# Performance work log

Hardware: AMD Instinct MI355X
Metric: run time of the kernel (lower is better)

The kernel has to match this reference:

```python
import jax, jax.numpy as jnp
import numpy as np

N, M, F0, FB, F, H, NC, NCONV = 60000, 12, 92, 41, 64, 128, 2000, 3
EPS = 1e-5


def setup_inputs() -> dict:
    key = jax.random.key(0)
    ks = jax.random.split(key, 12)
    s = 0.05
    return {
        "atom_fea": jax.random.normal(ks[0], (N, F0), jnp.float32),
        "nbr_fea": jax.random.normal(ks[1], (N, M, FB), jnp.float32),
        "nbr_fea_idx": jax.random.randint(ks[2], (N, M), 0, N),
        "crystal_atom_idx": jnp.sort(jax.random.randint(ks[3], (N,), 0, NC)),
        "W_emb": jax.random.normal(ks[4], (F0, F), jnp.float32) * s,
        "b_emb": jnp.zeros((F,), jnp.float32),
        "W_full": jax.random.normal(ks[5], (NCONV, 2 * F + FB, 2 * F), jnp.float32) * s,
        "b_full": jnp.zeros((NCONV, 2 * F), jnp.float32),
        "g1": jnp.ones((NCONV, 2 * F), jnp.float32),
        "be1": jnp.zeros((NCONV, 2 * F), jnp.float32),
        "g2": jnp.ones((NCONV, F), jnp.float32),
        "be2": jnp.zeros((NCONV, F), jnp.float32),
        "W_fc": jax.random.normal(ks[6], (F, H), jnp.float32) * s,
        "b_fc": jnp.zeros((H,), jnp.float32),
        "W_out": jax.random.normal(ks[7], (H, 1), jnp.float32) * s,
        "b_out": jnp.zeros((1,), jnp.float32),
    }


def _bn(x, g, b):
    # training-mode batch norm over leading (row) dim
    m = x.mean(axis=0)
    v = x.var(axis=0)
    return (x - m) * jax.lax.rsqrt(v + EPS) * g + b


def _conv_layer(x, nbr_fea, nbr_fea_idx, Wf, bf, g1, be1, g2, be2):
    n, m = nbr_fea_idx.shape
    f = x.shape[1]
    atom_nbr = x[nbr_fea_idx]  # (N, M, F) gather
    total = jnp.concatenate(
        [jnp.broadcast_to(x[:, None, :], (n, m, f)), atom_nbr, nbr_fea], axis=2
    )  # (N, M, 2F+FB)
    gated = total @ Wf + bf  # (N, M, 2F)
    gated = _bn(gated.reshape(-1, 2 * f), g1, be1).reshape(n, m, 2 * f)
    nbr_filter, nbr_core = jnp.split(gated, 2, axis=2)
    summed = jnp.sum(jax.nn.sigmoid(nbr_filter) * jax.nn.softplus(nbr_core), axis=1)
    summed = _bn(summed, g2, be2)
    return jax.nn.softplus(x + summed)


def reference(atom_fea, nbr_fea, nbr_fea_idx, crystal_atom_idx, W_emb, b_emb,
              W_full, b_full, g1, be1, g2, be2, W_fc, b_fc, W_out, b_out):
    x = atom_fea @ W_emb + b_emb  # (N, F)
    for i in range(NCONV):
        x = _conv_layer(x, nbr_fea, nbr_fea_idx, W_full[i], b_full[i],
                        g1[i], be1[i], g2[i], be2[i])
    # mean-pool atoms per crystal (segment mean)
    sums = jax.ops.segment_sum(x, crystal_atom_idx, num_segments=NC)
    cnt = jax.ops.segment_sum(jnp.ones((x.shape[0],), x.dtype), crystal_atom_idx,
                              num_segments=NC)
    crys = sums / jnp.maximum(cnt, 1.0)[:, None]  # (NC, F)
    crys = jax.nn.softplus(crys) @ W_fc + b_fc
    crys = jax.nn.softplus(crys)
    return crys @ W_out + b_out  # (NC, 1)
```

## Files before the change

### kernel.cpp

```cpp
#include <hip/hip_runtime.h>
#include <hip/hip_bf16.h>


#define NATOM 60000
#define MNBR  12
#define F0D   92
#define FBD   41
#define FD    64
#define F2D   128
#define NCRY  2000
#define HD    128
#define NSUP  15000
#define GS    132

#define OFF_X      0ull
#define OFF_XH     3840000ull
#define OFF_SUMMED 5760000ull
#define OFF_STATS  9600000ull
#define OFF_CRYS   9600384ull
#define OFF_CNT    9728384ull
#define OFF_WCONV  9730384ull
#define OFF_WBF    9811220ull
#define OFF_FLAG   9848084ull
#define WS_NEED_BYTES (9848085ull * 4ull)
#define OFF_BPAD   9848088ull
#define WS_FULL_BYTES ((OFF_BPAD + 17280000ull) * 4ull)

#define W_EMB_O  0
#define B_EMB_O  5888
#define W_FULL_O 5952
#define B_FULL_O 70848
#define G1_O     71232
#define BE1_O    71616
#define G2_O     72000
#define BE2_O    72192
#define W_FC_O   72384
#define B_FC_O   80576
#define W_OUT_O  80704
#define B_OUT_O  80832
#define WC_TOTAL 80833

typedef unsigned short u16;
typedef __attribute__((ext_vector_type(8))) short bf16x8;
typedef __attribute__((ext_vector_type(4))) float f32x4;

__device__ __forceinline__ float bf2f(u16 u){
  union { unsigned int i; float f; } v; v.i = ((unsigned int)u) << 16; return v.f;
}
__device__ __forceinline__ u16 f2bf(float f){
  union { float f; unsigned int i; } v; v.f = f;
  unsigned int x = v.i;
  return (u16)((x + 0x7FFFu + ((x >> 16) & 1u)) >> 16);
}
__device__ __forceinline__ float softplusf_(float x){
  return fmaxf(x, 0.f) + log1pf(expf(-fabsf(x)));
}
__device__ __forceinline__ float softplus_fast(float x){
  return fmaxf(x, 0.f) + __logf(1.f + __expf(-fabsf(x)));
}
__device__ __forceinline__ float sigmoid_fast(float x){
  return __builtin_amdgcn_rcpf(1.f + __expf(-x));
}

__global__ __launch_bounds__(64) void detect_kernel(
    const u16* __restrict__ data, int* __restrict__ flag){
  int tid = threadIdx.x;
  float v = bf2f(data[tid * 2]);
  float av = fabsf(v);
  bool sane = (av > 1e-6f) && (av < 100.f);
  unsigned long long m = __ballot(sane);
  if (tid == 0) *flag = (__popcll(m) >= 32) ? 1 : 0;
}

struct CvtArgs {
  const void* src[12];
  int start[13];
};

__global__ __launch_bounds__(256) void cvt_all_kernel(
    CvtArgs a, float* __restrict__ dst, const int* __restrict__ flag){
  int i = blockIdx.x * 256 + threadIdx.x;
  if (i >= WC_TOTAL) return;
  int r = 0;
  while (i >= a.start[r + 1]) r++;
  int rel = i - a.start[r];
  if (*flag) dst[i] = bf2f(((const u16*)a.src[r])[rel]);
  else       dst[i] = ((const float*)a.src[r])[rel];
}

__global__ __launch_bounds__(256) void build_bfrag(
    const float* __restrict__ wfull, u16* __restrict__ wbf){
  int t = blockIdx.x * 256 + threadIdx.x;
  if (t >= 3 * 6 * 8 * 64) return;
  int lane = t & 63, nt = (t >> 6) & 7, c = (t >> 9) % 6, layer = t / 3072;
  int q = lane >> 4, nloc = lane & 15;
  u16 vals[8];
  #pragma unroll
  for (int i = 0; i < 8; i++){
    int k = c * 32 + q * 8 + i;
    float v = (k < 169) ? wfull[layer * 169 * F2D + k * F2D + nt * 16 + nloc] : 0.f;
    vals[i] = f2bf(v);
  }
  *(uint4*)&wbf[(size_t)t * 8] = *(uint4*)vals;
}

__global__ __launch_bounds__(256) void bond_prep(
    const void* __restrict__ nbr_fea, u16* __restrict__ bond_pad,
    const int* __restrict__ flag){
  __shared__ __align__(16) char sm[7872];
  u16*   lb_u = (u16*)sm;
  float* lb_f = (float*)sm;
  int s = blockIdx.x, tid = threadIdx.x;
  const int isbf = *flag;
  if (isbf){
    const uint4* src = (const uint4*)((const u16*)nbr_fea + (size_t)s * 1968);
    if (tid < 246) ((uint4*)sm)[tid] = src[tid];
  } else {
    const uint4* src = (const uint4*)((const float*)nbr_fea + (size_t)s * 1968);
    for (int t = tid; t < 492; t += 256) ((uint4*)sm)[t] = src[t];
  }
  __syncthreads();
  uint4* outv = (uint4*)(bond_pad + (size_t)s * 2304);
  for (int slot = tid; slot < 288; slot += 256){
    int el = slot / 6, jj = slot - el * 6;
    u16 v[8];
    #pragma unroll
    for (int i = 0; i < 8; i++){
      int k = jj * 8 + i;
      v[i] = (k < FBD) ? (isbf ? lb_u[el * FBD + k] : f2bf(lb_f[el * FBD + k])) : (u16)0;
    }
    outv[slot] = *(uint4*)v;
  }
}

__global__ __launch_bounds__(256) void embed_kernel(
    const void* __restrict__ atom_fea, const float* __restrict__ W_emb,
    const float* __restrict__ b_emb, float* __restrict__ x,
    u16* __restrict__ xh, const int* __restrict__ flag){
  int tid = threadIdx.x;
  int n = blockIdx.x * 4 + (tid >> 6);
  int f = tid & 63;
  float acc = b_emb[f];
  if (*flag){
    const u16* arow = (const u16*)atom_fea + n * F0D;
    for (int k = 0; k < F0D; k++)
      acc = fmaf(bf2f(arow[k]), W_emb[k * FD + f], acc);
  } else {
    const float* arow = (const float*)atom_fea + n * F0D;
    for (int k = 0; k < F0D; k++)
      acc = fmaf(arow[k], W_emb[k * FD + f], acc);
  }
  x[n * FD + f] = acc;
  xh[n * FD + f] = f2bf(acc);
}

template<int ACT, int PAD>
__global__ __launch_bounds__(256, 3) void conv_mfma(
    const u16* __restrict__ xh, const void* __restrict__ nbr_fea,
    const u16* __restrict__ bond_pad,
    const int* __restrict__ nbr_idx, const u16* __restrict__ wbf_l,
    const float* __restrict__ bfull, const float* __restrict__ sum1,
    const float* __restrict__ sq1, const float* __restrict__ g1,
    const float* __restrict__ be1, float* __restrict__ summed,
    float* __restrict__ o_sum, float* __restrict__ o_sq,
    const int* __restrict__ flag){
  extern __shared__ char smem[];
  u16*   fragA = (u16*)smem;
  const int base_off = PAD ? 0 : 6144;
  float* gbuf  = (float*)(smem + base_off);
  float* redS  = ACT ? (gbuf + 48 * GS) : (float*)(smem + base_off);
  float* redQ  = redS + (ACT ? 64 : 128);

  const int tid = threadIdx.x;
  const int w = tid >> 6, lane = tid & 63;
  const int q = lane >> 4, nloc = lane & 15, q8 = q * 8;
  const int isbf = *flag;

  bf16x8 Bf[6][2];
  const bf16x8* Bv = (const bf16x8*)wbf_l;
  #pragma unroll
  for (int c = 0; c < 6; c++)
    #pragma unroll
    for (int t2 = 0; t2 < 2; t2++)
      Bf[c][t2] = Bv[(c * 8 + w * 2 + t2) * 64 + lane];
  float bias0 = bfull[w * 32 + nloc];
  float bias1 = bfull[w * 32 + 16 + nloc];

  float A0 = 0.f, B0 = 0.f, A1 = 0.f, B1 = 0.f;
  if (ACT){
    const float invR = 1.f / (float)(NATOM * MNBR);
    float m0 = sum1[lane] * invR;
    float v0 = fmaxf(sq1[lane] * invR - m0 * m0, 0.f);
    A0 = g1[lane] * rsqrtf(v0 + 1e-5f);  B0 = be1[lane] - m0 * A0;
    float m1 = sum1[64 + lane] * invR;
    float v1 = fmaxf(sq1[64 + lane] * invR - m1 * m1, 0.f);
    A1 = g1[64 + lane] * rsqrtf(v1 + 1e-5f);  B1 = be1[64 + lane] - m1 * A1;
  }
  float sAcc0 = 0.f, sAcc1 = 0.f, qAcc0 = 0.f, qAcc1 = 0.f;
  if (tid < (ACT ? 64 : 128)){ redS[tid] = 0.f; redQ[tid] = 0.f; }
  if (PAD && !ACT) ;

  const bf16x8* xv = (const bf16x8*)xh;
  const bf16x8 zero8 = {0,0,0,0,0,0,0,0};
  for (int s = blockIdx.x; s < NSUP; s += gridDim.x){
    int e0 = s * 48 + nloc;
    int nb0 = nbr_idx[e0], nb1 = nbr_idx[e0 + 16], nb2 = nbr_idx[e0 + 32];
    bf16x8 Af[3][6];
    if (PAD){
      #pragma unroll
      for (int et = 0; et < 3; et++){
        int nb = (et == 0) ? nb0 : (et == 1) ? nb1 : nb2;
        int na = s * 4 + (et * 16 + nloc) / 12;
        Af[et][0] = xv[na * 8 + q];
        Af[et][1] = xv[na * 8 + 4 + q];
        Af[et][2] = xv[nb * 8 + q];
        Af[et][3] = xv[nb * 8 + 4 + q];
        const bf16x8* bpv = (const bf16x8*)(bond_pad + (size_t)(e0 + et * 16) * 48);
        Af[et][4] = bpv[q];
        Af[et][5] = (q < 2) ? bpv[4 + q] : zero8;
      }
    } else {
      if (w < 3){
        size_t eg = (size_t)(s * 48 + w * 16 + nloc);
        u16 v4[8], v5[8];
        if (isbf){
          const u16* br = (const u16*)nbr_fea + eg * 41;
          #pragma unroll
          for (int i = 0; i < 8; i++) v4[i] = br[q8 + i];
          #pragma unroll
          for (int i = 0; i < 8; i++){
            int k5 = 32 + q8 + i;
            v5[i] = (k5 < 41) ? br[k5] : (u16)0;
          }
        } else {
          const float* br = (const float*)nbr_fea + eg * 41;
          #pragma unroll
          for (int i = 0; i < 8; i++) v4[i] = f2bf(br[q8 + i]);
          #pragma unroll
          for (int i = 0; i < 8; i++){
            int k5 = 32 + q8 + i;
            v5[i] = (k5 < 41) ? f2bf(br[k5]) : (u16)0;
          }
        }
        *(uint4*)&fragA[(w * 2 + 0) * 512 + lane * 8] = *(uint4*)v4;
        *(uint4*)&fragA[(w * 2 + 1) * 512 + lane * 8] = *(uint4*)v5;
      }
      __syncthreads();
      #pragma unroll
      for (int et = 0; et < 3; et++){
        int nb = (et == 0) ? nb0 : (et == 1) ? nb1 : nb2;
        int na = s * 4 + (et * 16 + nloc) / 12;
        Af[et][0] = xv[na * 8 + q];
        Af[et][1] = xv[na * 8 + 4 + q];
        Af[et][2] = xv[nb * 8 + q];
        Af[et][3] = xv[nb * 8 + 4 + q];
        Af[et][4] = *(bf16x8*)&fragA[(et * 2 + 0) * 512 + lane * 8];
        Af[et][5] = *(bf16x8*)&fragA[(et * 2 + 1) * 512 + lane * 8];
      }
    }
    #pragma unroll
    for (int et = 0; et < 3; et++){
      #pragma unroll
      for (int t2 = 0; t2 < 2; t2++){
        float bs = t2 ? bias1 : bias0;
        f32x4 acc = {bs, bs, bs, bs};
        acc = __builtin_amdgcn_mfma_f32_16x16x32_bf16(Af[et][0], Bf[0][t2], acc, 0, 0, 0);
        acc = __builtin_amdgcn_mfma_f32_16x16x32_bf16(Af[et][1], Bf[1][t2], acc, 0, 0, 0);
        acc = __builtin_amdgcn_mfma_f32_16x16x32_bf16(Af[et][2], Bf[2][t2], acc, 0, 0, 0);
        acc = __builtin_amdgcn_mfma_f32_16x16x32_bf16(Af[et][3], Bf[3][t2], acc, 0, 0, 0);
        acc = __builtin_amdgcn_mfma_f32_16x16x32_bf16(Af[et][4], Bf[4][t2], acc, 0, 0, 0);
        acc = __builtin_amdgcn_mfma_f32_16x16x32_bf16(Af[et][5], Bf[5][t2], acc, 0, 0, 0);
        if (ACT){
          int col = w * 32 + t2 * 16 + nloc;
          int r0 = et * 16 + q * 4;
          gbuf[(r0 + 0) * GS + col] = acc[0];
          gbuf[(r0 + 1) * GS + col] = acc[1];
          gbuf[(r0 + 2) * GS + col] = acc[2];
          gbuf[(r0 + 3) * GS + col] = acc[3];
        } else {
          float ss = acc[0] + acc[1] + acc[2] + acc[3];
          float qq = acc[0]*acc[0] + acc[1]*acc[1] + acc[2]*acc[2] + acc[3]*acc[3];
          if (t2){ sAcc1 += ss; qAcc1 += qq; } else { sAcc0 += ss; qAcc0 += qq; }
        }
      }
    }
    if (ACT){
      __syncthreads();
      float p = 0.f;
      #pragma unroll
      for (int m = 0; m < 12; m++){
        int el = w * 12 + m;
        float u = fmaf(gbuf[el * GS + lane],      A0, B0);
        float v = fmaf(gbuf[el * GS + 64 + lane], A1, B1);
        p = fmaf(sigmoid_fast(u), softplus_fast(v), p);
      }
      summed[(s * 4 + w) * 64 + lane] = p;
      sAcc0 += p;  qAcc0 = fmaf(p, p, qAcc0);
      __syncthreads();
    } else if (!PAD){
      __syncthreads();
    }
  }
  __syncthreads();
  if (ACT){
    atomicAdd(&redS[lane], sAcc0);
    atomicAdd(&redQ[lane], qAcc0);
    __syncthreads();
    if (tid < 64){ atomicAdd(&o_sum[tid], redS[tid]); atomicAdd(&o_sq[tid], redQ[tid]); }
  } else {
    int c0 = w * 32 + nloc;
    atomicAdd(&redS[c0], sAcc0);       atomicAdd(&redQ[c0], qAcc0);
    atomicAdd(&redS[c0 + 16], sAcc1);  atomicAdd(&redQ[c0 + 16], qAcc1);
    __syncthreads();
    if (tid < 128){ atomicAdd(&o_sum[tid], redS[tid]); atomicAdd(&o_sq[tid], redQ[tid]); }
  }
}

__global__ __launch_bounds__(256) void update_x_kernel(
    float* __restrict__ x, u16* __restrict__ xh,
    const float* __restrict__ summed,
    const float* __restrict__ sum2, const float* __restrict__ sq2,
    const float* __restrict__ g2, const float* __restrict__ be2){
  int idx = blockIdx.x * 256 + threadIdx.x;
  int f = idx & 63;
  const float invN = 1.f / (float)NATOM;
  float mean = sum2[f] * invN;
  float var  = fmaxf(sq2[f] * invN - mean * mean, 0.f);
  float a = g2[f] * rsqrtf(var + 1e-5f);
  float b = be2[f] - mean * a;
  float v = x[idx] + fmaf(summed[idx], a, b);
  float r = softplusf_(v);
  x[idx] = r;
  xh[idx] = f2bf(r);
}

__global__ __launch_bounds__(256) void pool_kernel(
    const float* __restrict__ x, const int* __restrict__ cidx,
    float* __restrict__ crys, float* __restrict__ cnt){
  int idx = blockIdx.x * 256 + threadIdx.x;
  int n = idx >> 6, f = idx & 63;
  int c = cidx[n];
  atomicAdd(&crys[c * FD + f], x[idx]);
  if (f == 0) atomicAdd(&cnt[c], 1.f);
}

__global__ __launch_bounds__(128) void head_kernel(
    const float* __restrict__ crys, const float* __restrict__ cnt,
    const float* __restrict__ W_fc, const float* __restrict__ b_fc,
    const float* __restrict__ W_out, const float* __restrict__ b_out,
    void* __restrict__ out, const int* __restrict__ flag){
  __shared__ float p_s[FD];
  __shared__ float red_s[HD];
  int c = blockIdx.x, tid = threadIdx.x;
  if (tid < FD){
    float ct = fmaxf(cnt[c], 1.f);
    p_s[tid] = softplusf_(crys[c * FD + tid] / ct);
  }
  __syncthreads();
  float acc = b_fc[tid];
  for (int k = 0; k < FD; k++)
    acc = fmaf(p_s[k], W_fc[k * HD + tid], acc);
  float h = softplusf_(acc);
  red_s[tid] = h * W_out[tid];
  __syncthreads();
  for (int s = HD / 2; s > 0; s >>= 1){
    if (tid < s) red_s[tid] += red_s[tid + s];
    __syncthreads();
  }
  if (tid == 0){
    float r = red_s[0] + b_out[0];
    if (*flag) ((u16*)out)[c] = f2bf(r);
    else       ((float*)out)[c] = r;
  }
}

extern "C" void kernel_launch(void* const* d_in, const int* in_sizes, int n_in,
                              void* d_out, int out_size, void* d_ws, size_t ws_size,
                              hipStream_t stream){
  if (ws_size < WS_NEED_BYTES) return;
  const bool full = (ws_size >= WS_FULL_BYTES);
  const void* atom_fea = d_in[0];
  const void* nbr_fea  = d_in[1];
  const int* nbr_idx   = (const int*)d_in[2];
  const int* cidx      = (const int*)d_in[3];

  float* ws     = (float*)d_ws;
  float* x      = ws + OFF_X;
  u16*   xh     = (u16*)(ws + OFF_XH);
  float* summed = ws + OFF_SUMMED;
  float* sum1   = ws + OFF_STATS;
  float* sq1    = sum1 + 128;
  float* sum2   = sq1 + 128;
  float* sq2    = sum2 + 64;
  float* crys   = ws + OFF_CRYS;
  float* cnt    = ws + OFF_CNT;
  float* wc     = ws + OFF_WCONV;
  u16*   wbf    = (u16*)(ws + OFF_WBF);
  int*   flag   = (int*)(ws + OFF_FLAG);
  u16*   bpad   = (u16*)(ws + OFF_BPAD);

  detect_kernel<<<1, 64, 0, stream>>>((const u16*)nbr_fea, flag);
  CvtArgs ca;
  const int srcidx[12] = {4,5,6,7,8,9,10,11,12,13,14,15};
  const int starts[13] = {W_EMB_O, B_EMB_O, W_FULL_O, B_FULL_O, G1_O, BE1_O,
                          G2_O, BE2_O, W_FC_O, B_FC_O, W_OUT_O, B_OUT_O, WC_TOTAL};
  for (int i = 0; i < 12; i++){ ca.src[i] = d_in[srcidx[i]]; ca.start[i] = starts[i]; }
  ca.start[12] = WC_TOTAL;
  cvt_all_kernel<<<(WC_TOTAL + 255) / 256, 256, 0, stream>>>(ca, wc, flag);
  build_bfrag<<<(9216 + 255) / 256, 256, 0, stream>>>(wc + W_FULL_O, wbf);
  if (full) bond_prep<<<NSUP, 256, 0, stream>>>(nbr_fea, bpad, flag);

  embed_kernel<<<NATOM / 4, 256, 0, stream>>>(atom_fea, wc + W_EMB_O, wc + B_EMB_O,
                                              x, xh, flag);
  const int LDS_STATS_P = 2 * 128 * 4;
  const int LDS_ACT_P   = (48 * GS + 128) * 4;
  const int LDS_STATS_F = 6144 + 2 * 128 * 4;
  const int LDS_ACT_F   = 6144 + (48 * GS + 128) * 4;
  for (int i = 0; i < 3; i++){
    const u16* wbf_l = wbf + (size_t)i * 3072 * 8;
    hipMemsetAsync(sum1, 0, 384 * sizeof(float), stream);
    if (full){
      conv_mfma<0,1><<<3000, 256, LDS_STATS_P, stream>>>(xh, nbr_fea, bpad, nbr_idx,
          wbf_l, wc + B_FULL_O + i * F2D, sum1, sq1, wc + G1_O + i * F2D,
          wc + BE1_O + i * F2D, summed, sum1, sq1, flag);
      conv_mfma<1,1><<<3000, 256, LDS_ACT_P, stream>>>(xh, nbr_fea, bpad, nbr_idx,
          wbf_l, wc + B_FULL_O + i * F2D, sum1, sq1, wc + G1_O + i * F2D,
          wc + BE1_O + i * F2D, summed, sum2, sq2, flag);
    } else {
      conv_mfma<0,0><<<3000, 256, LDS_STATS_F, stream>>>(xh, nbr_fea, bpad, nbr_idx,
          wbf_l, wc + B_FULL_O + i * F2D, sum1, sq1, wc + G1_O + i * F2D,
          wc + BE1_O + i * F2D, summed, sum1, sq1, flag);
      conv_mfma<1,0><<<3000, 256, LDS_ACT_F, stream>>>(xh, nbr_fea, bpad, nbr_idx,
          wbf_l, wc + B_FULL_O + i * F2D, sum1, sq1, wc + G1_O + i * F2D,
          wc + BE1_O + i * F2D, summed, sum2, sq2, flag);
    }
    update_x_kernel<<<(NATOM * FD) / 256, 256, 0, stream>>>(x, xh, summed, sum2, sq2,
        wc + G2_O + i * FD, wc + BE2_O + i * FD);
  }
  hipMemsetAsync(crys, 0, (NCRY * FD + NCRY) * sizeof(float), stream);
  pool_kernel<<<(NATOM * FD) / 256, 256, 0, stream>>>(x, cidx, crys, cnt);
  head_kernel<<<NCRY, 128, 0, stream>>>(crys, cnt, wc + W_FC_O, wc + B_FC_O,
      wc + W_OUT_O, wc + B_OUT_O, d_out, flag);
}
```

Before: 1.009 ms.

## Add software-pipelined 8-wave conv kernel with double-buffered register fragments

Adds a new conv kernel for the padded-bond path that runs 512 threads per block, with each wave owning one 16-column output tile. Each block handles exactly five super-tiles, with the neighbor indices loaded up front. Gather loads for the next group are double-buffered in registers so they overlap with the MFMAs of the current group, and sched_barrier pins the ordering. The activation phase is split across wave pairs through a small LDS partial buffer. This trades more barriers, a fixed grid-to-work mapping and higher register pressure for better latency hiding of the irregular gathers.

After: 1.359 ms. +34.6%, slower.

```diff
diff --git a/kernel.cpp b/kernel.cpp
--- a/kernel.cpp
+++ b/kernel.cpp
@@ -12,6 +12,7 @@
 #define HD    128
 #define NSUP  15000
 #define GS    132
+#define CGRID 3000
 
 #define OFF_X      0ull
 #define OFF_XH     3840000ull
@@ -154,10 +155,162 @@
   xh[n * FD + f] = f2bf(acc);
 }
 
-template<int ACT, int PAD>
+template<int ACT>
+__global__ __launch_bounds__(512, 4) void conv_pipe8(
+    const u16* __restrict__ xh, const u16* __restrict__ bond_pad,
+    const int* __restrict__ nbr_idx, const u16* __restrict__ wbf_l,
+    const float* __restrict__ bfull, const float* __restrict__ sum1,
+    const float* __restrict__ sq1, const float* __restrict__ g1,
+    const float* __restrict__ be1, float* __restrict__ summed,
+    float* __restrict__ o_sum, float* __restrict__ o_sq){
+  extern __shared__ char smem[];
+  float* gbuf = (float*)smem;
+  float* pbuf = gbuf + 48 * GS;
+  float* redS = ACT ? (pbuf + 4 * 64) : (float*)smem;
+  float* redQ = redS + (ACT ? 64 : 128);
+
+  const int tid = threadIdx.x;
+  const int wv = tid >> 6;
+  const int lane = tid & 63, q = lane >> 4, nloc = lane & 15;
+
+  bf16x8 Bf[6];
+  const bf16x8* Bv = (const bf16x8*)wbf_l;
+  #pragma unroll
+  for (int c = 0; c < 6; c++) Bf[c] = Bv[(c * 8 + wv) * 64 + lane];
+  const float bias = bfull[wv * 16 + nloc];
+
+  float A0 = 0.f, B0 = 0.f, A1 = 0.f, B1 = 0.f;
+  if (ACT){
+    const int cl = tid & 63;
+    const float invR = 1.f / (float)(NATOM * MNBR);
+    float m0 = sum1[cl] * invR;
+    float v0 = fmaxf(sq1[cl] * invR - m0 * m0, 0.f);
+    A0 = g1[cl] * rsqrtf(v0 + 1e-5f);  B0 = be1[cl] - m0 * A0;
+    float m1 = sum1[64 + cl] * invR;
+    float v1 = fmaxf(sq1[64 + cl] * invR - m1 * m1, 0.f);
+    A1 = g1[64 + cl] * rsqrtf(v1 + 1e-5f);  B1 = be1[64 + cl] - m1 * A1;
+  }
+  float sAcc = 0.f, qAcc = 0.f;
+  if (tid < (ACT ? 64 : 128)){ redS[tid] = 0.f; redQ[tid] = 0.f; }
+
+  const bf16x8* xv = (const bf16x8*)xh;
+  const char* bpad8 = (const char*)bond_pad;
+  const bf16x8 zero8 = {0,0,0,0,0,0,0,0};
+  const int s0 = blockIdx.x;
+
+  int nb[15];
+  #pragma unroll
+  for (int k = 0; k < 5; k++)
+    #pragma unroll
+    for (int et = 0; et < 3; et++)
+      nb[k * 3 + et] = nbr_idx[(s0 + k * CGRID) * 48 + et * 16 + nloc];
+
+  bf16x8 FA0, FA1, FA2, FA3, FA4, FA5;
+  bf16x8 FB0, FB1, FB2, FB3, FB4, FB5;
+
+#define LOADG(P, g_) {                                                          \
+    const int k_ = (g_) / 3, et_ = (g_) % 3;                                    \
+    const int ss_ = s0 + k_ * CGRID;                                            \
+    const int na_ = ss_ * 4 + (et_ * 16 + nloc) / 12;                           \
+    const int nb_ = nb[(g_)];                                                   \
+    P##0 = xv[(size_t)na_ * 8 + q];                                             \
+    P##1 = xv[(size_t)na_ * 8 + 4 + q];                                         \
+    P##2 = xv[(size_t)nb_ * 8 + q];                                             \
+    P##3 = xv[(size_t)nb_ * 8 + 4 + q];                                         \
+    const bf16x8* bp_ = (const bf16x8*)(bpad8 +                                 \
+        ((size_t)ss_ * 48 + et_ * 16 + nloc) * 96);                             \
+    P##4 = bp_[q];                                                              \
+    P##5 = (q < 2) ? bp_[4 + q] : zero8;                                        \
+  }
+
+#define MFMAG(P, g_) {                                                          \
+    const int et_ = (g_) % 3;                                                   \
+    f32x4 acc = {bias, bias, bias, bias};                                       \
+    acc = __builtin_amdgcn_mfma_f32_16x16x32_bf16(P##4, Bf[4], acc, 0, 0, 0);   \
+    acc = __builtin_amdgcn_mfma_f32_16x16x32_bf16(P##5, Bf[5], acc, 0, 0, 0);   \
+    acc = __builtin_amdgcn_mfma_f32_16x16x32_bf16(P##0, Bf[0], acc, 0, 0, 0);   \
+    acc = __builtin_amdgcn_mfma_f32_16x16x32_bf16(P##1, Bf[1], acc, 0, 0, 0);   \
+    acc = __builtin_amdgcn_mfma_f32_16x16x32_bf16(P##2, Bf[2], acc, 0, 0, 0);   \
+    acc = __builtin_amdgcn_mfma_f32_16x16x32_bf16(P##3, Bf[3], acc, 0, 0, 0);   \
+    if (ACT){                                                                   \
+      const int col_ = wv * 16 + nloc;                                          \
+      const int r0_ = et_ * 16 + q * 4;                                         \
+      gbuf[(r0_ + 0) * GS + col_] = acc[0];                                     \
+      gbuf[(r0_ + 1) * GS + col_] = acc[1];                                     \
+      gbuf[(r0_ + 2) * GS + col_] = acc[2];                                     \
+      gbuf[(r0_ + 3) * GS + col_] = acc[3];                                     \
+    } else {                                                                    \
+      sAcc += acc[0] + acc[1] + acc[2] + acc[3];                                \
+      qAcc += acc[0]*acc[0] + acc[1]*acc[1] + acc[2]*acc[2] + acc[3]*acc[3];    \
+    }                                                                           \
+  }
+
+#define STEP(P, g_) { MFMAG(P, g_); LOADG(P, (g_) + 2);                         \
+    __builtin_amdgcn_sched_barrier(0); }
+#define STEPL(P, g_) { MFMAG(P, g_); __builtin_amdgcn_sched_barrier(0); }
+
+#define ACTPH(k_) if (ACT){                                                     \
+    __builtin_amdgcn_sched_barrier(0);                                          \
+    asm volatile("s_waitcnt lgkmcnt(0)");                                       \
+    __builtin_amdgcn_s_barrier();                                               \
+    __builtin_amdgcn_sched_barrier(0);                                          \
+    const int cl_ = tid & 63, a_ = tid >> 7, h_ = (tid >> 6) & 1;               \
+    float ph = 0.f;                                                             \
+    _Pragma("unroll")                                                           \
+    for (int m = 0; m < 6; m++){                                                \
+      int el = a_ * 12 + h_ * 6 + m;                                            \
+      float u = fmaf(gbuf[el * GS + cl_],      A0, B0);                         \
+      float v = fmaf(gbuf[el * GS + 64 + cl_], A1, B1);                         \
+      ph = fmaf(sigmoid_fast(u), softplus_fast(v), ph);                         \
+    }                                                                           \
+    if (h_) pbuf[a_ * 64 + cl_] = ph;                                           \
+    __builtin_amdgcn_sched_barrier(0);                                          \
+    asm volatile("s_waitcnt lgkmcnt(0)");                                       \
+    __builtin_amdgcn_s_barrier();                                               \
+    __builtin_amdgcn_sched_barrier(0);                                          \
+    if (!h_){                                                                   \
+      float p = ph + pbuf[a_ * 64 + cl_];                                       \
+      summed[((size_t)(s0 + (k_) * CGRID) * 4 + a_) * 64 + cl_] = p;            \
+      sAcc += p;  qAcc = fmaf(p, p, qAcc);                                      \
+    }                                                                           \
+  }
+
+  LOADG(FA, 0);
+  LOADG(FB, 1);
+  __builtin_amdgcn_sched_barrier(0);
+
+  STEP(FA, 0);  STEP(FB, 1);  STEP(FA, 2);   ACTPH(0);
+  STEP(FB, 3);  STEP(FA, 4);  STEP(FB, 5);   ACTPH(1);
+  STEP(FA, 6);  STEP(FB, 7);  STEP(FA, 8);   ACTPH(2);
+  STEP(FB, 9);  STEP(FA, 10); STEP(FB, 11);  ACTPH(3);
+  STEP(FA, 12); STEPL(FB, 13); STEPL(FA, 14); ACTPH(4);
+
+#undef LOADG
+#undef MFMAG
+#undef STEP
+#undef STEPL
+#undef ACTPH
+
+  __syncthreads();
+  if (ACT){
+    if (!((tid >> 6) & 1)){
+      atomicAdd(&redS[tid & 63], sAcc);
+      atomicAdd(&redQ[tid & 63], qAcc);
+    }
+    __syncthreads();
+    if (tid < 64){ atomicAdd(&o_sum[tid], redS[tid]); atomicAdd(&o_sq[tid], redQ[tid]); }
+  } else {
+    int c0 = wv * 16 + nloc;
+    atomicAdd(&redS[c0], sAcc);
+    atomicAdd(&redQ[c0], qAcc);
+    __syncthreads();
+    if (tid < 128){ atomicAdd(&o_sum[tid], redS[tid]); atomicAdd(&o_sq[tid], redQ[tid]); }
+  }
+}
+
+template<int ACT>
 __global__ __launch_bounds__(256, 3) void conv_mfma(
     const u16* __restrict__ xh, const void* __restrict__ nbr_fea,
-    const u16* __restrict__ bond_pad,
     const int* __restrict__ nbr_idx, const u16* __restrict__ wbf_l,
     const float* __restrict__ bfull, const float* __restrict__ sum1,
     const float* __restrict__ sq1, const float* __restrict__ g1,
@@ -166,9 +319,8 @@
     const int* __restrict__ flag){
   extern __shared__ char smem[];
   u16*   fragA = (u16*)smem;
-  const int base_off = PAD ? 0 : 6144;
-  float* gbuf  = (float*)(smem + base_off);
-  float* redS  = ACT ? (gbuf + 48 * GS) : (float*)(smem + base_off);
+  float* gbuf  = (float*)(smem + 6144);
+  float* redS  = ACT ? (gbuf + 48 * GS) : (float*)(smem + 6144);
   float* redQ  = redS + (ACT ? 64 : 128);
 
   const int tid = threadIdx.x;
@@ -198,65 +350,48 @@
   }
   float sAcc0 = 0.f, sAcc1 = 0.f, qAcc0 = 0.f, qAcc1 = 0.f;
   if (tid < (ACT ? 64 : 128)){ redS[tid] = 0.f; redQ[tid] = 0.f; }
-  if (PAD && !ACT) ;
 
   const bf16x8* xv = (const bf16x8*)xh;
-  const bf16x8 zero8 = {0,0,0,0,0,0,0,0};
   for (int s = blockIdx.x; s < NSUP; s += gridDim.x){
     int e0 = s * 48 + nloc;
     int nb0 = nbr_idx[e0], nb1 = nbr_idx[e0 + 16], nb2 = nbr_idx[e0 + 32];
     bf16x8 Af[3][6];
-    if (PAD){
-      #pragma unroll
-      for (int et = 0; et < 3; et++){
-        int nb = (et == 0) ? nb0 : (et == 1) ? nb1 : nb2;
-        int na = s * 4 + (et * 16 + nloc) / 12;
-        Af[et][0] = xv[na * 8 + q];
-        Af[et][1] = xv[na * 8 + 4 + q];
-        Af[et][2] = xv[nb * 8 + q];
-        Af[et][3] = xv[nb * 8 + 4 + q];
-        const bf16x8* bpv = (const bf16x8*)(bond_pad + (size_t)(e0 + et * 16) * 48);
-        Af[et][4] = bpv[q];
-        Af[et][5] = (q < 2) ? bpv[4 + q] : zero8;
+    if (w < 3){
+      size_t eg = (size_t)(s * 48 + w * 16 + nloc);
+      u16 v4[8], v5[8];
+      if (isbf){
+        const u16* br = (const u16*)nbr_fea + eg * 41;
+        #pragma unroll
+        for (int i = 0; i < 8; i++) v4[i] = br[q8 + i];
+        #pragma unroll
+        for (int i = 0; i < 8; i++){
+          int k5 = 32 + q8 + i;
+          v5[i] = (k5 < 41) ? br[k5] : (u16)0;
+        }
+      } else {
+        const float* br = (const float*)nbr_fea + eg * 41;
+        #pragma unroll
+        for (int i = 0; i < 8; i++) v4[i] = f2bf(br[q8 + i]);
+        #pragma unroll
+        for (int i = 0; i < 8; i++){
+          int k5 = 32 + q8 + i;
+          v5[i] = (k5 < 41) ? f2bf(br[k5]) : (u16)0;
+        }
       }
-    } else {
-      if (w < 3){
-        size_t eg = (size_t)(s * 48 + w * 16 + nloc);
-        u16 v4[8], v5[8];
-        if (isbf){
-          const u16* br = (const u16*)nbr_fea + eg * 41;
-          #pragma unroll
-          for (int i = 0; i < 8; i++) v4[i] = br[q8 + i];
-          #pragma unroll
-          for (int i = 0; i < 8; i++){
-            int k5 = 32 + q8 + i;
-            v5[i] = (k5 < 41) ? br[k5] : (u16)0;
-          }
-        } else {
-          const float* br = (const float*)nbr_fea + eg * 41;
-          #pragma unroll
-          for (int i = 0; i < 8; i++) v4[i] = f2bf(br[q8 + i]);
-          #pragma unroll
-          for (int i = 0; i < 8; i++){
-            int k5 = 32 + q8 + i;
-            v5[i] = (k5 < 41) ? f2bf(br[k5]) : (u16)0;
-          }
-        }
-        *(uint4*)&fragA[(w * 2 + 0) * 512 + lane * 8] = *(uint4*)v4;
-        *(uint4*)&fragA[(w * 2 + 1) * 512 + lane * 8] = *(uint4*)v5;
-      }
-      __syncthreads();
-      #pragma unroll
-      for (int et = 0; et < 3; et++){
-        int nb = (et == 0) ? nb0 : (et == 1) ? nb1 : nb2;
-        int na = s * 4 + (et * 16 + nloc) / 12;
-        Af[et][0] = xv[na * 8 + q];
-        Af[et][1] = xv[na * 8 + 4 + q];
-        Af[et][2] = xv[nb * 8 + q];
-        Af[et][3] = xv[nb * 8 + 4 + q];
-        Af[et][4] = *(bf16x8*)&fragA[(et * 2 + 0) * 512 + lane * 8];
-        Af[et][5] = *(bf16x8*)&fragA[(et * 2 + 1) * 512 + lane * 8];
-      }
+      *(uint4*)&fragA[(w * 2 + 0) * 512 + lane * 8] = *(uint4*)v4;
+      *(uint4*)&fragA[(w * 2 + 1) * 512 + lane * 8] = *(uint4*)v5;
+    }
+    __syncthreads();
+    #pragma unroll
+    for (int et = 0; et < 3; et++){
+      int nb = (et == 0) ? nb0 : (et == 1) ? nb1 : nb2;
+      int na = s * 4 + (et * 16 + nloc) / 12;
+      Af[et][0] = xv[na * 8 + q];
+      Af[et][1] = xv[na * 8 + 4 + q];
+      Af[et][2] = xv[nb * 8 + q];
+      Af[et][3] = xv[nb * 8 + 4 + q];
+      Af[et][4] = *(bf16x8*)&fragA[(et * 2 + 0) * 512 + lane * 8];
+      Af[et][5] = *(bf16x8*)&fragA[(et * 2 + 1) * 512 + lane * 8];
     }
     #pragma unroll
     for (int et = 0; et < 3; et++){
@@ -296,12 +431,9 @@
       }
       summed[(s * 4 + w) * 64 + lane] = p;
       sAcc0 += p;  qAcc0 = fmaf(p, p, qAcc0);
-      __syncthreads();
-    } else if (!PAD){
-      __syncthreads();
-    }
-  }
-  __syncthreads();
+    }
+    __syncthreads();
+  }
   if (ACT){
     atomicAdd(&redS[lane], sAcc0);
     atomicAdd(&redQ[lane], qAcc0);
@@ -413,24 +545,24 @@
   embed_kernel<<<NATOM / 4, 256, 0, stream>>>(atom_fea, wc + W_EMB_O, wc + B_EMB_O,
                                               x, xh, flag);
   const int LDS_STATS_P = 2 * 128 * 4;
-  const int LDS_ACT_P   = (48 * GS + 128) * 4;
+  const int LDS_ACT_P   = (48 * GS + 4 * 64 + 2 * 64) * 4;
   const int LDS_STATS_F = 6144 + 2 * 128 * 4;
   const int LDS_ACT_F   = 6144 + (48 * GS + 128) * 4;
   for (int i = 0; i < 3; i++){
     const u16* wbf_l = wbf + (size_t)i * 3072 * 8;
     hipMemsetAsync(sum1, 0, 384 * sizeof(float), stream);
     if (full){
-      conv_mfma<0,1><<<3000, 256, LDS_STATS_P, stream>>>(xh, nbr_fea, bpad, nbr_idx,
+      conv_pipe8<0><<<CGRID, 512, LDS_STATS_P, stream>>>(xh, bpad, nbr_idx,
+          wbf_l, wc + B_FULL_O + i * F2D, sum1, sq1, wc + G1_O + i * F2D,
+          wc + BE1_O + i * F2D, summed, sum1, sq1);
+      conv_pipe8<1><<<CGRID, 512, LDS_ACT_P, stream>>>(xh, bpad, nbr_idx,
+          wbf_l, wc + B_FULL_O + i * F2D, sum1, sq1, wc + G1_O + i * F2D,
+          wc + BE1_O + i * F2D, summed, sum2, sq2);
+    } else {
+      conv_mfma<0><<<CGRID, 256, LDS_STATS_F, stream>>>(xh, nbr_fea, nbr_idx,
           wbf_l, wc + B_FULL_O + i * F2D, sum1, sq1, wc + G1_O + i * F2D,
           wc + BE1_O + i * F2D, summed, sum1, sq1, flag);
-      conv_mfma<1,1><<<3000, 256, LDS_ACT_P, stream>>>(xh, nbr_fea, bpad, nbr_idx,
-          wbf_l, wc + B_FULL_O + i * F2D, sum1, sq1, wc + G1_O + i * F2D,
-          wc + BE1_O + i * F2D, summed, sum2, sq2, flag);
-    } else {
-      conv_mfma<0,0><<<3000, 256, LDS_STATS_F, stream>>>(xh, nbr_fea, bpad, nbr_idx,
-          wbf_l, wc + B_FULL_O + i * F2D, sum1, sq1, wc + G1_O + i * F2D,
-          wc + BE1_O + i * F2D, summed, sum1, sq1, flag);
-      conv_mfma<1,0><<<3000, 256, LDS_ACT_F, stream>>>(xh, nbr_fea, bpad, nbr_idx,
+      conv_mfma<1><<<CGRID, 256, LDS_ACT_F, stream>>>(xh, nbr_fea, nbr_idx,
           wbf_l, wc + B_FULL_O + i * F2D, sum1, sq1, wc + G1_O + i * F2D,
           wc + BE1_O + i * F2D, summed, sum2, sq2, flag);
     }
```

## Add 512-thread conv kernel with per-wave column split and prefetched neighbor indices

Applied to the files above, without the earlier changes.

Adds a new conv_batch kernel for the padded-bond path. It runs 8 waves per block, each owning 16 output columns instead of 32, so each wave holds fewer B fragments and does less MFMA work per supertile. Neighbor indices for the next iteration are prefetched, loads are issued before an asm barrier to batch memory traffic, and the activation reduction is split across two half-waves through an LDS partial buffer. The cost is that the A fragments (x rows and bond features) are loaded redundantly by all 8 waves, and the ACT path needs extra barriers.

Measured after the change: 1.485 ms. +47.1%, slower.

```diff
diff --git a/kernel.cpp b/kernel.cpp
--- a/kernel.cpp
+++ b/kernel.cpp
@@ -12,6 +12,7 @@
 #define HD    128
 #define NSUP  15000
 #define GS    132
+#define CGRID 3000
 
 #define OFF_X      0ull
 #define OFF_XH     3840000ull
@@ -154,10 +155,157 @@
   xh[n * FD + f] = f2bf(acc);
 }
 
-template<int ACT, int PAD>
+template<int ACT>
+__global__ __launch_bounds__(512) void conv_batch(
+    const u16* __restrict__ xh, const u16* __restrict__ bond_pad,
+    const int* __restrict__ nbr_idx, const u16* __restrict__ wbf_l,
+    const float* __restrict__ bfull, const float* __restrict__ sum1,
+    const float* __restrict__ sq1, const float* __restrict__ g1,
+    const float* __restrict__ be1, float* __restrict__ summed,
+    float* __restrict__ o_sum, float* __restrict__ o_sq){
+  extern __shared__ char smem[];
+  float* gbuf = (float*)smem;
+  float* pbuf = gbuf + 48 * GS;
+  float* redS = ACT ? (pbuf + 4 * 64) : (float*)smem;
+  float* redQ = redS + (ACT ? 64 : 128);
+
+  const int tid = threadIdx.x;
+  const int wv = tid >> 6;
+  const int lane = tid & 63, q = lane >> 4, nloc = lane & 15;
+
+  bf16x8 Bf[6];
+  const bf16x8* Bv = (const bf16x8*)wbf_l;
+  #pragma unroll
+  for (int c = 0; c < 6; c++) Bf[c] = Bv[(c * 8 + wv) * 64 + lane];
+  const float bias = bfull[wv * 16 + nloc];
+
+  float A0 = 0.f, B0 = 0.f, A1 = 0.f, B1 = 0.f;
+  if (ACT){
+    const int cl = tid & 63;
+    const float invR = 1.f / (float)(NATOM * MNBR);
+    float m0 = sum1[cl] * invR;
+    float v0 = fmaxf(sq1[cl] * invR - m0 * m0, 0.f);
+    A0 = g1[cl] * rsqrtf(v0 + 1e-5f);  B0 = be1[cl] - m0 * A0;
+    float m1 = sum1[64 + cl] * invR;
+    float v1 = fmaxf(sq1[64 + cl] * invR - m1 * m1, 0.f);
+    A1 = g1[64 + cl] * rsqrtf(v1 + 1e-5f);  B1 = be1[64 + cl] - m1 * A1;
+  }
+  float sAcc = 0.f, qAcc = 0.f;
+  if (tid < (ACT ? 64 : 128)){ redS[tid] = 0.f; redQ[tid] = 0.f; }
+
+  const int na_off0 = nloc / 12;
+  const int na_off1 = (16 + nloc) / 12;
+  const int na_off2 = (32 + nloc) / 12;
+
+  const bf16x8* xv = (const bf16x8*)xh;
+  const bf16x8 zero8 = {0,0,0,0,0,0,0,0};
+  const int s0 = blockIdx.x;
+
+  int nbc0 = nbr_idx[s0 * 48 + nloc];
+  int nbc1 = nbr_idx[s0 * 48 + 16 + nloc];
+  int nbc2 = nbr_idx[s0 * 48 + 32 + nloc];
+
+  #pragma unroll 1
+  for (int k = 0; k < 5; k++){
+    const int s = s0 + k * CGRID;
+    const size_t e0 = (size_t)s * 48 + nloc;
+    const bf16x8* bp0 = (const bf16x8*)(bond_pad + e0 * 48);
+    const bf16x8* bp1 = (const bf16x8*)(bond_pad + (e0 + 16) * 48);
+    const bf16x8* bp2 = (const bf16x8*)(bond_pad + (e0 + 32) * 48);
+    bf16x8 d00 = bp0[q], d01 = (q < 2) ? bp0[4 + q] : zero8;
+    bf16x8 d10 = bp1[q], d11 = (q < 2) ? bp1[4 + q] : zero8;
+    bf16x8 d20 = bp2[q], d21 = (q < 2) ? bp2[4 + q] : zero8;
+    const int na0 = s * 4 + na_off0, na1 = s * 4 + na_off1, na2 = s * 4 + na_off2;
+    bf16x8 x00 = xv[(size_t)na0 * 8 + q],   x01 = xv[(size_t)na0 * 8 + 4 + q];
+    bf16x8 x02 = xv[(size_t)nbc0 * 8 + q],  x03 = xv[(size_t)nbc0 * 8 + 4 + q];
+    bf16x8 x10 = xv[(size_t)na1 * 8 + q],   x11 = xv[(size_t)na1 * 8 + 4 + q];
+    bf16x8 x12 = xv[(size_t)nbc1 * 8 + q],  x13 = xv[(size_t)nbc1 * 8 + 4 + q];
+    bf16x8 x20 = xv[(size_t)na2 * 8 + q],   x21 = xv[(size_t)na2 * 8 + 4 + q];
+    bf16x8 x22 = xv[(size_t)nbc2 * 8 + q],  x23 = xv[(size_t)nbc2 * 8 + 4 + q];
+    if (k < 4){
+      nbc0 = nbr_idx[(s + CGRID) * 48 + nloc];
+      nbc1 = nbr_idx[(s + CGRID) * 48 + 16 + nloc];
+      nbc2 = nbr_idx[(s + CGRID) * 48 + 32 + nloc];
+    }
+    asm volatile("" :
+      "+v"(d00), "+v"(d01), "+v"(d10), "+v"(d11), "+v"(d20), "+v"(d21),
+      "+v"(x00), "+v"(x01), "+v"(x02), "+v"(x03),
+      "+v"(x10), "+v"(x11), "+v"(x12), "+v"(x13),
+      "+v"(x20), "+v"(x21), "+v"(x22), "+v"(x23));
+    #pragma unroll
+    for (int et = 0; et < 3; et++){
+      bf16x8 b0_ = (et == 0) ? d00 : (et == 1) ? d10 : d20;
+      bf16x8 b1_ = (et == 0) ? d01 : (et == 1) ? d11 : d21;
+      bf16x8 a0_ = (et == 0) ? x00 : (et == 1) ? x10 : x20;
+      bf16x8 a1_ = (et == 0) ? x01 : (et == 1) ? x11 : x21;
+      bf16x8 a2_ = (et == 0) ? x02 : (et == 1) ? x12 : x22;
+      bf16x8 a3_ = (et == 0) ? x03 : (et == 1) ? x13 : x23;
+      f32x4 acc = {bias, bias, bias, bias};
+      acc = __builtin_amdgcn_mfma_f32_16x16x32_bf16(b0_, Bf[4], acc, 0, 0, 0);
+      acc = __builtin_amdgcn_mfma_f32_16x16x32_bf16(b1_, Bf[5], acc, 0, 0, 0);
+      acc = __builtin_amdgcn_mfma_f32_16x16x32_bf16(a0_, Bf[0], acc, 0, 0, 0);
+      acc = __builtin_amdgcn_mfma_f32_16x16x32_bf16(a1_, Bf[1], acc, 0, 0, 0);
+      acc = __builtin_amdgcn_mfma_f32_16x16x32_bf16(a2_, Bf[2], acc, 0, 0, 0);
+      acc = __builtin_amdgcn_mfma_f32_16x16x32_bf16(a3_, Bf[3], acc, 0, 0, 0);
+      if (ACT){
+        const int col = wv * 16 + nloc;
+        const int r0 = et * 16 + q * 4;
+        gbuf[(r0 + 0) * GS + col] = acc[0];
+        gbuf[(r0 + 1) * GS + col] = acc[1];
+        gbuf[(r0 + 2) * GS + col] = acc[2];
+        gbuf[(r0 + 3) * GS + col] = acc[3];
+      } else {
+        sAcc += acc[0] + acc[1] + acc[2] + acc[3];
+        qAcc += acc[0]*acc[0] + acc[1]*acc[1] + acc[2]*acc[2] + acc[3]*acc[3];
+      }
+    }
+    if (ACT){
+      __builtin_amdgcn_sched_barrier(0);
+      asm volatile("s_waitcnt lgkmcnt(0)");
+      __builtin_amdgcn_s_barrier();
+      __builtin_amdgcn_sched_barrier(0);
+      const int cl = tid & 63, a = tid >> 7, h = (tid >> 6) & 1;
+      float ph = 0.f;
+      #pragma unroll
+      for (int m = 0; m < 6; m++){
+        int el = a * 12 + h * 6 + m;
+        float u = fmaf(gbuf[el * GS + cl],      A0, B0);
+        float v = fmaf(gbuf[el * GS + 64 + cl], A1, B1);
+        ph = fmaf(sigmoid_fast(u), softplus_fast(v), ph);
+      }
+      if (h) pbuf[a * 64 + cl] = ph;
+      __builtin_amdgcn_sched_barrier(0);
+      asm volatile("s_waitcnt lgkmcnt(0)");
+      __builtin_amdgcn_s_barrier();
+      __builtin_amdgcn_sched_barrier(0);
+      if (!h){
+        float p = ph + pbuf[a * 64 + cl];
+        summed[((size_t)s * 4 + a) * 64 + cl] = p;
+        sAcc += p;  qAcc = fmaf(p, p, qAcc);
+      }
+    }
+  }
+
+  __syncthreads();
+  if (ACT){
+    if (!((tid >> 6) & 1)){
+      atomicAdd(&redS[tid & 63], sAcc);
+      atomicAdd(&redQ[tid & 63], qAcc);
+    }
+    __syncthreads();
+    if (tid < 64){ atomicAdd(&o_sum[tid], redS[tid]); atomicAdd(&o_sq[tid], redQ[tid]); }
+  } else {
+    int c0 = wv * 16 + nloc;
+    atomicAdd(&redS[c0], sAcc);
+    atomicAdd(&redQ[c0], qAcc);
+    __syncthreads();
+    if (tid < 128){ atomicAdd(&o_sum[tid], redS[tid]); atomicAdd(&o_sq[tid], redQ[tid]); }
+  }
+}
+
+template<int ACT>
 __global__ __launch_bounds__(256, 3) void conv_mfma(
     const u16* __restrict__ xh, const void* __restrict__ nbr_fea,
-    const u16* __restrict__ bond_pad,
     const int* __restrict__ nbr_idx, const u16* __restrict__ wbf_l,
     const float* __restrict__ bfull, const float* __restrict__ sum1,
     const float* __restrict__ sq1, const float* __restrict__ g1,
@@ -166,9 +314,8 @@
     const int* __restrict__ flag){
   extern __shared__ char smem[];
   u16*   fragA = (u16*)smem;
-  const int base_off = PAD ? 0 : 6144;
-  float* gbuf  = (float*)(smem + base_off);
-  float* redS  = ACT ? (gbuf + 48 * GS) : (float*)(smem + base_off);
+  float* gbuf  = (float*)(smem + 6144);
+  float* redS  = ACT ? (gbuf + 48 * GS) : (float*)(smem + 6144);
   float* redQ  = redS + (ACT ? 64 : 128);
 
   const int tid = threadIdx.x;
@@ -198,65 +345,48 @@
   }
   float sAcc0 = 0.f, sAcc1 = 0.f, qAcc0 = 0.f, qAcc1 = 0.f;
   if (tid < (ACT ? 64 : 128)){ redS[tid] = 0.f; redQ[tid] = 0.f; }
-  if (PAD && !ACT) ;
 
   const bf16x8* xv = (const bf16x8*)xh;
-  const bf16x8 zero8 = {0,0,0,0,0,0,0,0};
   for (int s = blockIdx.x; s < NSUP; s += gridDim.x){
     int e0 = s * 48 + nloc;
     int nb0 = nbr_idx[e0], nb1 = nbr_idx[e0 + 16], nb2 = nbr_idx[e0 + 32];
     bf16x8 Af[3][6];
-    if (PAD){
-      #pragma unroll
-      for (int et = 0; et < 3; et++){
-        int nb = (et == 0) ? nb0 : (et == 1) ? nb1 : nb2;
-        int na = s * 4 + (et * 16 + nloc) / 12;
-        Af[et][0] = xv[na * 8 + q];
-        Af[et][1] = xv[na * 8 + 4 + q];
-        Af[et][2] = xv[nb * 8 + q];
-        Af[et][3] = xv[nb * 8 + 4 + q];
-        const bf16x8* bpv = (const bf16x8*)(bond_pad + (size_t)(e0 + et * 16) * 48);
-        Af[et][4] = bpv[q];
-        Af[et][5] = (q < 2) ? bpv[4 + q] : zero8;
+    if (w < 3){
+      size_t eg = (size_t)(s * 48 + w * 16 + nloc);
+      u16 v4[8], v5[8];
+      if (isbf){
+        const u16* br = (const u16*)nbr_fea + eg * 41;
+        #pragma unroll
+        for (int i = 0; i < 8; i++) v4[i] = br[q8 + i];
+        #pragma unroll
+        for (int i = 0; i < 8; i++){
+          int k5 = 32 + q8 + i;
+          v5[i] = (k5 < 41) ? br[k5] : (u16)0;
+        }
+      } else {
+        const float* br = (const float*)nbr_fea + eg * 41;
+        #pragma unroll
+        for (int i = 0; i < 8; i++) v4[i] = f2bf(br[q8 + i]);
+        #pragma unroll
+        for (int i = 0; i < 8; i++){
+          int k5 = 32 + q8 + i;
+          v5[i] = (k5 < 41) ? f2bf(br[k5]) : (u16)0;
+        }
       }
-    } else {
-      if (w < 3){
-        size_t eg = (size_t)(s * 48 + w * 16 + nloc);
-        u16 v4[8], v5[8];
-        if (isbf){
-          const u16* br = (const u16*)nbr_fea + eg * 41;
-          #pragma unroll
-          for (int i = 0; i < 8; i++) v4[i] = br[q8 + i];
-          #pragma unroll
-          for (int i = 0; i < 8; i++){
-            int k5 = 32 + q8 + i;
-            v5[i] = (k5 < 41) ? br[k5] : (u16)0;
-          }
-        } else {
-          const float* br = (const float*)nbr_fea + eg * 41;
-          #pragma unroll
-          for (int i = 0; i < 8; i++) v4[i] = f2bf(br[q8 + i]);
-          #pragma unroll
-          for (int i = 0; i < 8; i++){
-            int k5 = 32 + q8 + i;
-            v5[i] = (k5 < 41) ? f2bf(br[k5]) : (u16)0;
-          }
-        }
-        *(uint4*)&fragA[(w * 2 + 0) * 512 + lane * 8] = *(uint4*)v4;
-        *(uint4*)&fragA[(w * 2 + 1) * 512 + lane * 8] = *(uint4*)v5;
-      }
-      __syncthreads();
-      #pragma unroll
-      for (int et = 0; et < 3; et++){
-        int nb = (et == 0) ? nb0 : (et == 1) ? nb1 : nb2;
-        int na = s * 4 + (et * 16 + nloc) / 12;
-        Af[et][0] = xv[na * 8 + q];
-        Af[et][1] = xv[na * 8 + 4 + q];
-        Af[et][2] = xv[nb * 8 + q];
-        Af[et][3] = xv[nb * 8 + 4 + q];
-        Af[et][4] = *(bf16x8*)&fragA[(et * 2 + 0) * 512 + lane * 8];
-        Af[et][5] = *(bf16x8*)&fragA[(et * 2 + 1) * 512 + lane * 8];
-      }
+      *(uint4*)&fragA[(w * 2 + 0) * 512 + lane * 8] = *(uint4*)v4;
+      *(uint4*)&fragA[(w * 2 + 1) * 512 + lane * 8] = *(uint4*)v5;
+    }
+    __syncthreads();
+    #pragma unroll
+    for (int et = 0; et < 3; et++){
+      int nb = (et == 0) ? nb0 : (et == 1) ? nb1 : nb2;
+      int na = s * 4 + (et * 16 + nloc) / 12;
+      Af[et][0] = xv[na * 8 + q];
+      Af[et][1] = xv[na * 8 + 4 + q];
+      Af[et][2] = xv[nb * 8 + q];
+      Af[et][3] = xv[nb * 8 + 4 + q];
+      Af[et][4] = *(bf16x8*)&fragA[(et * 2 + 0) * 512 + lane * 8];
+      Af[et][5] = *(bf16x8*)&fragA[(et * 2 + 1) * 512 + lane * 8];
     }
     #pragma unroll
     for (int et = 0; et < 3; et++){
@@ -296,12 +426,9 @@
       }
       summed[(s * 4 + w) * 64 + lane] = p;
       sAcc0 += p;  qAcc0 = fmaf(p, p, qAcc0);
-      __syncthreads();
-    } else if (!PAD){
-      __syncthreads();
-    }
-  }
-  __syncthreads();
+    }
+    __syncthreads();
+  }
   if (ACT){
     atomicAdd(&redS[lane], sAcc0);
     atomicAdd(&redQ[lane], qAcc0);
@@ -412,25 +539,25 @@
 
   embed_kernel<<<NATOM / 4, 256, 0, stream>>>(atom_fea, wc + W_EMB_O, wc + B_EMB_O,
                                               x, xh, flag);
-  const int LDS_STATS_P = 2 * 128 * 4;
-  const int LDS_ACT_P   = (48 * GS + 128) * 4;
+  const int LDS_STATS_B = 2 * 128 * 4;
+  const int LDS_ACT_B   = (48 * GS + 4 * 64 + 2 * 64) * 4;
   const int LDS_STATS_F = 6144 + 2 * 128 * 4;
   const int LDS_ACT_F   = 6144 + (48 * GS + 128) * 4;
   for (int i = 0; i < 3; i++){
     const u16* wbf_l = wbf + (size_t)i * 3072 * 8;
     hipMemsetAsync(sum1, 0, 384 * sizeof(float), stream);
     if (full){
-      conv_mfma<0,1><<<3000, 256, LDS_STATS_P, stream>>>(xh, nbr_fea, bpad, nbr_idx,
+      conv_batch<0><<<CGRID, 512, LDS_STATS_B, stream>>>(xh, bpad, nbr_idx,
+          wbf_l, wc + B_FULL_O + i * F2D, sum1, sq1, wc + G1_O + i * F2D,
+          wc + BE1_O + i * F2D, summed, sum1, sq1);
+      conv_batch<1><<<CGRID, 512, LDS_ACT_B, stream>>>(xh, bpad, nbr_idx,
+          wbf_l, wc + B_FULL_O + i * F2D, sum1, sq1, wc + G1_O + i * F2D,
+          wc + BE1_O + i * F2D, summed, sum2, sq2);
+    } else {
+      conv_mfma<0><<<CGRID, 256, LDS_STATS_F, stream>>>(xh, nbr_fea, nbr_idx,
           wbf_l, wc + B_FULL_O + i * F2D, sum1, sq1, wc + G1_O + i * F2D,
           wc + BE1_O + i * F2D, summed, sum1, sq1, flag);
-      conv_mfma<1,1><<<3000, 256, LDS_ACT_P, stream>>>(xh, nbr_fea, bpad, nbr_idx,
-          wbf_l, wc + B_FULL_O + i * F2D, sum1, sq1, wc + G1_O + i * F2D,
-          wc + BE1_O + i * F2D, summed, sum2, sq2, flag);
-    } else {
-      conv_mfma<0,0><<<3000, 256, LDS_STATS_F, stream>>>(xh, nbr_fea, bpad, nbr_idx,
-          wbf_l, wc + B_FULL_O + i * F2D, sum1, sq1, wc + G1_O + i * F2D,
-          wc + BE1_O + i * F2D, summed, sum1, sq1, flag);
-      conv_mfma<1,0><<<3000, 256, LDS_ACT_F, stream>>>(xh, nbr_fea, bpad, nbr_idx,
+      conv_mfma<1><<<CGRID, 256, LDS_ACT_F, stream>>>(xh, nbr_fea, nbr_idx,
           wbf_l, wc + B_FULL_O + i * F2D, sum1, sq1, wc + G1_O + i * F2D,
           wc + BE1_O + i * F2D, summed, sum2, sq2, flag);
     }
```
